# Kernel tuning notes

Measured on AMD Instinct MI355X. Metric: run time of the kernel, lower is better.

## Reference

```python
import jax, jax.numpy as jnp
import numpy as np

NUM_HEADS = 16
MAX_BATCH = 4
MAX_SEQ = 2048


def setup_inputs() -> dict:
    key = jax.random.key(0)
    ks = jax.random.split(key, 9)
    B, S, H = 4, 2048, 2048
    scale = 0.02
    hidden_state = jax.random.normal(ks[0], (B, S, H), dtype=jnp.float32)
    # causal mask (masked_fill where mask == 0), broadcastable over batch/heads
    mask = jnp.tril(jnp.ones((S, S), dtype=jnp.int32))[None, None]  # [1,1,S,S]
    Wq = jax.random.normal(ks[1], (H, H), dtype=jnp.float32) * scale
    Wk = jax.random.normal(ks[2], (H, H), dtype=jnp.float32) * scale
    Wv = jax.random.normal(ks[3], (H, H), dtype=jnp.float32) * scale
    Wo = jax.random.normal(ks[4], (H, H), dtype=jnp.float32) * scale
    bq = jax.random.normal(ks[5], (H,), dtype=jnp.float32) * scale
    bk = jax.random.normal(ks[6], (H,), dtype=jnp.float32) * scale
    bv = jax.random.normal(ks[7], (H,), dtype=jnp.float32) * scale
    bo = jax.random.normal(ks[8], (H,), dtype=jnp.float32) * scale
    return {"hidden_state": hidden_state, "mask": mask,
            "Wq": Wq, "bq": bq, "Wk": Wk, "bk": bk,
            "Wv": Wv, "bv": bv, "Wo": Wo, "bo": bo,
            "start_pos": 0}


def reference(hidden_state, mask, Wq, bq, Wk, bk, Wv, bv, Wo, bo, start_pos):
    B, S, H = hidden_state.shape
    nh = NUM_HEADS
    hd = H // nh
    # qkv projections (nn.Linear: x @ W.T + b)
    q = (hidden_state @ Wq.T + bq).reshape(B, S, nh, hd)
    k = (hidden_state @ Wk.T + bk).reshape(B, S, nh, hd)
    v = (hidden_state @ Wv.T + bv).reshape(B, S, nh, hd)
    # KV-cache append (zeros-initialized buffer, write [start_pos:start_pos+S])
    cache_k = jnp.zeros((MAX_BATCH, MAX_SEQ, nh, hd), dtype=q.dtype)
    cache_v = jnp.zeros((MAX_BATCH, MAX_SEQ, nh, hd), dtype=q.dtype)
    cache_k = jax.lax.dynamic_update_slice(cache_k, k, (0, start_pos, 0, 0))
    cache_v = jax.lax.dynamic_update_slice(cache_v, v, (0, start_pos, 0, 0))
    total = start_pos + S
    key = cache_k[:B, :total]   # [B, total, nh, hd]
    value = cache_v[:B, :total]
    # scores: [B, nh, S, total]
    scores = jnp.einsum('bqhd,bkhd->bhqk', q, key) / jnp.sqrt(jnp.float32(hd))
    scores = jnp.where(mask == 0, -jnp.inf, scores)
    probs = jax.nn.softmax(scores, axis=-1)
    out = jnp.einsum('bhqk,bkhd->bqhd', probs, value).reshape(B, S, H)
    return out @ Wo.T + bo
```

## Files before the change

kernel.cpp:

```cpp
#include <hip/hip_runtime.h>
#include <hip/hip_bf16.h>
#include <stdint.h>

#define S_LEN 2048
#define HDIM  2048
#define NH    16
#define HD    128
#define BATCH 4

typedef __attribute__((ext_vector_type(8))) short bf16x8;
typedef __attribute__((ext_vector_type(4))) float f32x4;
typedef __attribute__((ext_vector_type(4))) float float4v;
typedef __attribute__((ext_vector_type(4))) unsigned short u16x4;

__device__ __forceinline__ void gload_lds16(const void* g, void* l) {
  __builtin_amdgcn_global_load_lds(
      (const __attribute__((address_space(1))) unsigned int*)g,
      (__attribute__((address_space(3))) unsigned int*)l,
      16, 0, 0);
}

__device__ __forceinline__ unsigned short f2bf(float x) {
  __hip_bfloat16 b = __float2bfloat16(x);
  return *reinterpret_cast<unsigned short*>(&b);
}

#define SL2E 0.1275174465f

__global__ __launch_bounds__(256) void cvt5_kernel(
    const float* __restrict__ x,
    const float* __restrict__ w0, const float* __restrict__ w1,
    const float* __restrict__ w2, const float* __restrict__ w3,
    unsigned short* __restrict__ ox,
    unsigned short* __restrict__ o0, unsigned short* __restrict__ o1,
    unsigned short* __restrict__ o2, unsigned short* __restrict__ o3,
    int n4x, int n4w) {
  const int y = blockIdx.y;
  const float* in = (y == 0) ? x : (y == 1) ? w0 : (y == 2) ? w1 : (y == 3) ? w2 : w3;
  unsigned short* out = (y == 0) ? ox : (y == 1) ? o0 : (y == 2) ? o1 : (y == 3) ? o2 : o3;
  const int n4 = (y == 0) ? n4x : n4w;
  int stride = gridDim.x * blockDim.x;
  for (int i = blockIdx.x * blockDim.x + threadIdx.x; i < n4; i += stride) {
    float4v v = *(const float4v*)(in + (size_t)i * 4);
    u16x4 o;
    o.x = f2bf(v.x); o.y = f2bf(v.y); o.z = f2bf(v.z); o.w = f2bf(v.w);
    *(u16x4*)(out + (size_t)i * 4) = o;
  }
}


#define G8_VMW(N) asm volatile("s_waitcnt vmcnt(" #N ")" ::: "memory")
#define G8_BAR1() do { __builtin_amdgcn_sched_barrier(0); __builtin_amdgcn_s_barrier(); \
  asm volatile("s_waitcnt lgkmcnt(0)" ::: "memory"); __builtin_amdgcn_sched_barrier(0); } while (0)
#define G8_BAR2() do { __builtin_amdgcn_sched_barrier(0); __builtin_amdgcn_s_barrier(); \
  __builtin_amdgcn_sched_barrier(0); } while (0)

#define G8_STAGE(ISB, BUF, HALF, KT) do {                                          \
  int kt_ = (KT); if (kt_ > nkt1) kt_ = nkt1;                                      \
  const char* gs_ = ((ISB) ? Bg : Ag) +                                            \
      (size_t)(((ISB) ? bn : bm) * 256 + (HALF) * 128 + w * 16) * (size_t)K2 +     \
      (size_t)kt_ * 128;                                                           \
  char* ld_ = lds + (BUF) * 65536 + (ISB) * 32768 + ((HALF) * 128 + w * 16) * 128; \
  gload_lds16(gs_ + sLn, ld_);                                                     \
  gload_lds16(gs_ + 8 * (size_t)K2 + sLn, ld_ + 1024);                             \
} while (0)

#define G8_RDA(BUF, MI0) do {                                                      \
  _Pragma("unroll") for (int mi = 0; mi < 4; ++mi)                                 \
  _Pragma("unroll") for (int kk = 0; kk < 2; ++kk)                                 \
    a[mi][kk] = *(const bf16x8*)(lds + (BUF) * 65536 +                             \
        (wm + ((MI0) + mi) * 16 + ln) * 128 + ((((kk << 2) + g) ^ ln7) << 4));     \
} while (0)

#define G8_RDB(BUF, NI0, BREG) do {                                                \
  _Pragma("unroll") for (int ni = 0; ni < 2; ++ni)                                 \
  _Pragma("unroll") for (int kk = 0; kk < 2; ++kk)                                 \
    BREG[ni][kk] = *(const bf16x8*)(lds + (BUF) * 65536 + 32768 +                  \
        (wn + ((NI0) + ni) * 16 + ln) * 128 + ((((kk << 2) + g) ^ ln7) << 4));     \
} while (0)

#define G8_MFMA(M0, N0, BREG) do {                                                 \
  __builtin_amdgcn_s_setprio(1);                                                   \
  _Pragma("unroll") for (int mi = 0; mi < 4; ++mi)                                 \
  _Pragma("unroll") for (int ni = 0; ni < 2; ++ni)                                 \
  _Pragma("unroll") for (int kk = 0; kk < 2; ++kk)                                 \
    acc[(M0) + mi][(N0) + ni] = __builtin_amdgcn_mfma_f32_16x16x32_bf16(           \
        a[mi][kk], BREG[ni][kk], acc[(M0) + mi][(N0) + ni], 0, 0, 0);              \
  __builtin_amdgcn_s_setprio(0);                                                   \
} while (0)

#define G8_MAIN_LOOP() do {                                                        \
  G8_STAGE(0, 0, 0, 0); G8_STAGE(0, 0, 1, 0);                                      \
  G8_STAGE(1, 0, 0, 0); G8_STAGE(1, 0, 1, 0);                                      \
  G8_STAGE(1, 1, 0, 1); G8_STAGE(1, 1, 1, 1);                                      \
  G8_VMW(4);                                                                       \
  G8_BAR2();                                                                       \
  for (int i = 0; i < niter; ++i) {                                                \
    const int v = 2 * i + 1, u2 = 2 * i + 2, v2 = 2 * i + 3;                       \
    bf16x8 a[4][2], b0[2][2], b1[2][2];                                            \
    G8_RDA(0, 0); G8_RDB(0, 0, b0);                                                \
    G8_STAGE(0, 1, 0, v);                                                          \
    G8_BAR1(); G8_MFMA(0, 0, b0); G8_BAR2();                                       \
    G8_RDB(0, 2, b1);                                                              \
    G8_STAGE(0, 1, 1, v);                                                          \
    G8_BAR1(); G8_MFMA(0, 2, b1); G8_BAR2();                                       \
    G8_RDA(0, 4);                                                                  \
    G8_STAGE(1, 0, 0, u2);                                                         \
    G8_BAR1(); G8_MFMA(4, 0, b0); G8_BAR2();                                       \
    G8_STAGE(1, 0, 1, u2);                                                         \
    G8_VMW(4);                                                                     \
    G8_BAR1(); G8_MFMA(4, 2, b1); G8_BAR2();                                       \
    G8_RDA(1, 0); G8_RDB(1, 0, b0);                                                \
    G8_STAGE(0, 0, 0, u2);                                                         \
    G8_BAR1(); G8_MFMA(0, 0, b0); G8_BAR2();                                       \
    G8_RDB(1, 2, b1);                                                              \
    G8_STAGE(0, 0, 1, u2);                                                         \
    G8_BAR1(); G8_MFMA(0, 2, b1); G8_BAR2();                                       \
    G8_RDA(1, 4);                                                                  \
    G8_STAGE(1, 1, 0, v2);                                                         \
    G8_BAR1(); G8_MFMA(4, 0, b0); G8_BAR2();                                       \
    G8_STAGE(1, 1, 1, v2);                                                         \
    G8_VMW(4);                                                                     \
    G8_BAR1(); G8_MFMA(4, 2, b1); G8_BAR2();                                       \
  }                                                                                \
  G8_VMW(0);                                                                       \
} while (0)

__global__ __launch_bounds__(512, 2) void gemm8_qkv(
    const __hip_bfloat16* __restrict__ A,
    const __hip_bfloat16* __restrict__ Bq, const __hip_bfloat16* __restrict__ Bk,
    const __hip_bfloat16* __restrict__ Bv,
    const float* __restrict__ biasq, const float* __restrict__ biask,
    const float* __restrict__ biasv,
    __hip_bfloat16* __restrict__ Cq, __hip_bfloat16* __restrict__ Ck,
    __hip_bfloat16* __restrict__ Cv,
    int M, int N, int K) {
  __shared__ char lds[131072];
  const int tid = threadIdx.x;
  const int w = tid >> 6;
  const int lane = tid & 63;
  const int g = lane >> 4;
  const int ln = lane & 15;
  const int ln7 = lane & 7;
  const int K2 = K * 2;
  const int nkt = K >> 6;
  const int nkt1 = nkt - 1;
  const int niter = nkt >> 1;

  const int proj = blockIdx.x >> 8;
  const int bid  = blockIdx.x & 255;
  const int NBN = N >> 8;
  const int cpx = ((M >> 8) * NBN) >> 3;
  const int wg = (bid & 7) * cpx + (bid >> 3);
  const int bm = wg / NBN, bn = wg % NBN;

  const int wm = (w >> 2) * 128;
  const int wn = (w & 3) * 64;

  const char* Ag = (const char*)A;
  const char* Bg = (proj == 0) ? (const char*)Bq : (proj == 1) ? (const char*)Bk
                                                               : (const char*)Bv;
  const float* bias = (proj == 0) ? biasq : (proj == 1) ? biask : biasv;
  const float scale = (proj == 0) ? SL2E : 1.0f;
  const size_t sLn = (size_t)(lane >> 3) * (size_t)K2 +
                     (size_t)(((lane & 7) ^ (lane >> 3)) << 4);

  f32x4 acc[8][4];
#pragma unroll
  for (int mi = 0; mi < 8; ++mi)
#pragma unroll
    for (int ni = 0; ni < 4; ++ni) acc[mi][ni] = (f32x4){0.f, 0.f, 0.f, 0.f};

  G8_MAIN_LOOP();

#pragma unroll
  for (int ni = 0; ni < 4; ++ni) {
    const int col = bn * 256 + wn + ni * 16 + ln;
    const float bv = bias[col];
#pragma unroll
    for (int mi = 0; mi < 8; ++mi) {
      const int row0 = bm * 256 + wm + mi * 16 + g * 4;
      if (proj == 2) {
        const int h = col >> 7, d = col & 127;
        const size_t base = ((size_t)((row0 >> 11) * NH + h) * HD + d) * S_LEN +
                            (row0 & (S_LEN - 1));
        u16x4 pk;
#pragma unroll
        for (int r = 0; r < 4; ++r) pk[r] = f2bf(acc[mi][ni][r] + bv);
        *(u16x4*)((unsigned short*)Cv + base) = pk;
      } else {
        __hip_bfloat16* C = (proj == 0) ? Cq : Ck;
#pragma unroll
        for (int r = 0; r < 4; ++r)
          C[(size_t)(row0 + r) * N + col] = __float2bfloat16((acc[mi][ni][r] + bv) * scale);
      }
    }
  }
}

template<int OUTMODE>
__global__ __launch_bounds__(512, 2) void gemm8(
    const __hip_bfloat16* __restrict__ A, const __hip_bfloat16* __restrict__ B,
    const float* __restrict__ bias, void* __restrict__ C,
    int M, int N, int K, float scale) {
  __shared__ char lds[131072];
  const int tid = threadIdx.x;
  const int w = tid >> 6;
  const int lane = tid & 63;
  const int g = lane >> 4;
  const int ln = lane & 15;
  const int ln7 = lane & 7;
  const int K2 = K * 2;
  const int nkt = K >> 6;
  const int nkt1 = nkt - 1;
  const int niter = nkt >> 1;

  const int NBN = N >> 8;
  const int nwg = (M >> 8) * NBN;
  const int cpx = nwg >> 3;
  const int bid = blockIdx.x;
  const int wg = (bid & 7) * cpx + (bid >> 3);
  const int bm = wg / NBN, bn = wg % NBN;

  const int wm = (w >> 2) * 128;
  const int wn = (w & 3) * 64;

  const char* Ag = (const char*)A;
  const char* Bg = (const char*)B;
  const size_t sLn = (size_t)(lane >> 3) * (size_t)K2 +
                     (size_t)(((lane & 7) ^ (lane >> 3)) << 4);

  f32x4 acc[8][4];
#pragma unroll
  for (int mi = 0; mi < 8; ++mi)
#pragma unroll
    for (int ni = 0; ni < 4; ++ni) acc[mi][ni] = (f32x4){0.f, 0.f, 0.f, 0.f};

  G8_MAIN_LOOP();

#pragma unroll
  for (int ni = 0; ni < 4; ++ni) {
    const int col = bn * 256 + wn + ni * 16 + ln;
    const float bv = bias[col];
#pragma unroll
    for (int mi = 0; mi < 8; ++mi) {
      const int row0 = bm * 256 + wm + mi * 16 + g * 4;
#pragma unroll
      for (int r = 0; r < 4; ++r) {
        float val = (acc[mi][ni][r] + bv) * scale;
        if (OUTMODE == 1)
          ((float*)C)[(size_t)(row0 + r) * N + col] = val;
        else
          ((__hip_bfloat16*)C)[(size_t)(row0 + r) * N + col] = __float2bfloat16(val);
      }
    }
  }
}

#define DEFER_THR 8.0f

__global__ __launch_bounds__(256, 2) void attn_kernel(
    const __hip_bfloat16* __restrict__ Q, const __hip_bfloat16* __restrict__ Kg,
    const __hip_bfloat16* __restrict__ Vt, __hip_bfloat16* __restrict__ O) {
  __shared__ char lds[49152];
  const int tid = threadIdx.x;
  const int w = tid >> 6;
  const int lane = tid & 63;
  const int g = lane >> 4;
  const int ln = lane & 15;
  const int bh = blockIdx.x;
  const int pairid = blockIdx.y;
  const int b = bh >> 4, h = bh & 15;

  const char* Qb = (const char*)Q + ((size_t)b * S_LEN * HDIM + h * HD) * 2;
  const char* Kb = (const char*)Kg + ((size_t)b * S_LEN * HDIM + h * HD) * 2;
  const char* Vb = (const char*)Vt + ((size_t)bh * HD * S_LEN) * 2;
  char* ldsK = lds;
  char* ldsV = lds + 16384;
  char* pw   = lds + 32768 + w * 4096;

  const int kr = lane >> 4;
  const int kc = lane & 15;
  const int vr = lane >> 3;
  const int vc = lane & 7;

  auto stage = [&](int kv0) {
#pragma unroll
    for (int i = 0; i < 4; i++) {
      int r = w * 16 + i * 4 + kr;
      gload_lds16(Kb + (size_t)(kv0 + r) * (HDIM * 2) + ((kc ^ (r & 7)) << 4),
                  ldsK + (w * 16 + i * 4) * 256);
    }
#pragma unroll
    for (int i = 0; i < 4; i++) {
      int r = w * 32 + i * 8 + vr;
      gload_lds16(Vb + (size_t)r * (S_LEN * 2) + (size_t)kv0 * 2 + ((vc ^ vr) << 4),
                  ldsV + (w * 32 + i * 8) * 128);
    }
  };

  for (int pass = 0; pass < 2; pass++) {
    const int qt = pass == 0 ? (15 - pairid) : pairid;
    const int q0 = qt * 128 + w * 32;

    const int nt = 2 * qt + 2;
    __syncthreads();
    stage(0);

    bf16x8 qf[2][4];
#pragma unroll
    for (int qs = 0; qs < 2; qs++)
#pragma unroll
      for (int dc = 0; dc < 4; dc++)
        qf[qs][dc] = *(const bf16x8*)(Qb + (size_t)(q0 + qs * 16 + ln) * HDIM * 2 +
                                      (dc * 32 + g * 8) * 2);

    f32x4 o[2][8];
#pragma unroll
    for (int qs = 0; qs < 2; qs++)
#pragma unroll
      for (int ds = 0; ds < 8; ds++) o[qs][ds] = (f32x4){0.f, 0.f, 0.f, 0.f};
    float mrun[2][4], lrun[2][4];
#pragma unroll
    for (int qs = 0; qs < 2; qs++)
#pragma unroll
      for (int r = 0; r < 4; r++) { mrun[qs][r] = -__builtin_inff(); lrun[qs][r] = 0.f; }

    __syncthreads();

    for (int t = 0; t < nt; t++) {
      const int kv0 = t * 64;

      if (kv0 <= q0 + 31) {
        f32x4 sa[2][4];
#pragma unroll
        for (int qs = 0; qs < 2; qs++)
#pragma unroll
          for (int ks = 0; ks < 4; ks++) sa[qs][ks] = (f32x4){0.f, 0.f, 0.f, 0.f};
#pragma unroll
        for (int dc = 0; dc < 4; dc++) {
          bf16x8 kf[4];
#pragma unroll
          for (int ks = 0; ks < 4; ks++)
            kf[ks] = *(const bf16x8*)(ldsK + (ks * 16 + ln) * 256 +
                                      (((dc * 4 + g) ^ (ln & 7)) << 4));
          __builtin_amdgcn_s_setprio(1);
#pragma unroll
          for (int qs = 0; qs < 2; qs++)
#pragma unroll
            for (int ks = 0; ks < 4; ks++)
              sa[qs][ks] = __builtin_amdgcn_mfma_f32_16x16x32_bf16(qf[qs][dc], kf[ks], sa[qs][ks], 0, 0, 0);
          __builtin_amdgcn_s_setprio(0);
        }
        const bool needmask = (kv0 + 63) > q0;
        if (needmask) {
#pragma unroll
          for (int qs = 0; qs < 2; qs++)
#pragma unroll
            for (int ks = 0; ks < 4; ks++)
#pragma unroll
              for (int r = 0; r < 4; r++)
                if ((kv0 + ks * 16 + ln) > (q0 + qs * 16 + g * 4 + r))
                  sa[qs][ks][r] = -__builtin_inff();
        }
        float pmax[2][4];
#pragma unroll
        for (int qs = 0; qs < 2; qs++)
#pragma unroll
          for (int r = 0; r < 4; r++) {
            float mx = fmaxf(fmaxf(sa[qs][0][r], sa[qs][1][r]), fmaxf(sa[qs][2][r], sa[qs][3][r]));
            mx = fmaxf(mx, __shfl_xor(mx, 1));
            mx = fmaxf(mx, __shfl_xor(mx, 2));
            mx = fmaxf(mx, __shfl_xor(mx, 4));
            mx = fmaxf(mx, __shfl_xor(mx, 8));
            pmax[qs][r] = mx;
          }
        float dmin = 1e30f;
#pragma unroll
        for (int qs = 0; qs < 2; qs++)
#pragma unroll
          for (int r = 0; r < 4; r++)
            dmin = fminf(dmin, mrun[qs][r] + DEFER_THR - pmax[qs][r]);
        if (!__all(dmin >= 0.0f)) {
          float alpha[2][4];
#pragma unroll
          for (int qs = 0; qs < 2; qs++)
#pragma unroll
            for (int r = 0; r < 4; r++) {
              float mn = fmaxf(mrun[qs][r], pmax[qs][r]);
              alpha[qs][r] = exp2f(mrun[qs][r] - mn);
              mrun[qs][r] = mn;
              lrun[qs][r] *= alpha[qs][r];
            }
#pragma unroll
          for (int qs = 0; qs < 2; qs++)
#pragma unroll
            for (int ds = 0; ds < 8; ds++)
#pragma unroll
              for (int r = 0; r < 4; r++) o[qs][ds][r] *= alpha[qs][r];
        }
        float rsum[2][4];
#pragma unroll
        for (int qs = 0; qs < 2; qs++)
#pragma unroll
          for (int r = 0; r < 4; r++) rsum[qs][r] = 0.f;
#pragma unroll
        for (int qs = 0; qs < 2; qs++)
#pragma unroll
          for (int ks = 0; ks < 4; ks++)
#pragma unroll
            for (int r = 0; r < 4; r++) {
              float p = exp2f(sa[qs][ks][r] - mrun[qs][r]);
              sa[qs][ks][r] = p;
              rsum[qs][r] += p;
            }
#pragma unroll
        for (int qs = 0; qs < 2; qs++)
#pragma unroll
          for (int r = 0; r < 4; r++) {
            float rs = rsum[qs][r];
            rs += __shfl_xor(rs, 1);
            rs += __shfl_xor(rs, 2);
            rs += __shfl_xor(rs, 4);
            rs += __shfl_xor(rs, 8);
            lrun[qs][r] += rs;
          }
#pragma unroll
        for (int qs = 0; qs < 2; qs++)
#pragma unroll
          for (int ks = 0; ks < 4; ks++)
#pragma unroll
            for (int r = 0; r < 4; r++) {
              int row = qs * 16 + g * 4 + r;
              int key = ks * 16 + ln;
              *(__hip_bfloat16*)(pw + row * 128 + (((key >> 3) ^ (row & 7)) << 4) + (key & 7) * 2) =
                  __float2bfloat16(sa[qs][ks][r]);
            }
#pragma unroll
        for (int kk = 0; kk < 2; kk++) {
          bf16x8 pa[2];
#pragma unroll
          for (int qs = 0; qs < 2; qs++) {
            int row = qs * 16 + ln;
            pa[qs] = *(const bf16x8*)(pw + row * 128 + (((kk * 4 + g) ^ (row & 7)) << 4));
          }
          __builtin_amdgcn_s_setprio(1);
#pragma unroll
          for (int ds = 0; ds < 8; ds++) {
            bf16x8 vf = *(const bf16x8*)(ldsV + (ds * 16 + ln) * 128 +
                                         (((kk * 4 + g) ^ (ln & 7)) << 4));
#pragma unroll
            for (int qs = 0; qs < 2; qs++)
              o[qs][ds] = __builtin_amdgcn_mfma_f32_16x16x32_bf16(pa[qs], vf, o[qs][ds], 0, 0, 0);
          }
          __builtin_amdgcn_s_setprio(0);
        }
      }

      if (t + 1 < nt) {
        __syncthreads();
        stage(kv0 + 64);
        __syncthreads();
      }
    }
    float inv[2][4];
#pragma unroll
    for (int qs = 0; qs < 2; qs++)
#pragma unroll
      for (int r = 0; r < 4; r++) inv[qs][r] = 1.0f / lrun[qs][r];
    __hip_bfloat16* Ob = O + (size_t)b * S_LEN * HDIM + h * HD;
#pragma unroll
    for (int qs = 0; qs < 2; qs++)
#pragma unroll
      for (int ds = 0; ds < 8; ds++)
#pragma unroll
        for (int r = 0; r < 4; r++)
          Ob[(size_t)(q0 + qs * 16 + g * 4 + r) * HDIM + ds * 16 + ln] =
              __float2bfloat16(o[qs][ds][r] * inv[qs][r]);
  }
}

extern "C" void kernel_launch(void* const* d_in, const int* in_sizes, int n_in,
                              void* d_out, int out_size, void* d_ws, size_t ws_size,
                              hipStream_t stream) {
  const float* X  = (const float*)d_in[0];
  const float* Wq = (const float*)d_in[2];
  const float* bq = (const float*)d_in[3];
  const float* Wk = (const float*)d_in[4];
  const float* bk = (const float*)d_in[5];
  const float* Wv = (const float*)d_in[6];
  const float* bv = (const float*)d_in[7];
  const float* Wo = (const float*)d_in[8];
  const float* bo = (const float*)d_in[9];

  char* ws = (char*)d_ws;
  __hip_bfloat16* Xb   = (__hip_bfloat16*)(ws);
  __hip_bfloat16* Wqb  = (__hip_bfloat16*)(ws + 33554432);
  __hip_bfloat16* Wkb  = (__hip_bfloat16*)(ws + 41943040);
  __hip_bfloat16* Wvb  = (__hip_bfloat16*)(ws + 50331648);
  __hip_bfloat16* Wob  = (__hip_bfloat16*)(ws + 58720256);
  __hip_bfloat16* Qb   = (__hip_bfloat16*)(ws + 67108864);
  __hip_bfloat16* Kb   = (__hip_bfloat16*)(ws + 100663296);
  __hip_bfloat16* Ob   = (__hip_bfloat16*)(ws + 134217728);
  __hip_bfloat16* Vtb  = (__hip_bfloat16*)(ws + 167772160);

  cvt5_kernel<<<dim3(512, 5), 256, 0, stream>>>(
      X, Wq, Wk, Wv, Wo,
      (unsigned short*)Xb,
      (unsigned short*)Wqb, (unsigned short*)Wkb,
      (unsigned short*)Wvb, (unsigned short*)Wob,
      16777216 / 4, 4194304 / 4);

  gemm8_qkv<<<768, 512, 0, stream>>>(Xb, Wqb, Wkb, Wvb, bq, bk, bv,
                                     Qb, Kb, Vtb, 8192, 2048, 2048);

  attn_kernel<<<dim3(64, 8), 256, 0, stream>>>(Qb, Kb, Vtb, Ob);

  gemm8<1><<<256, 512, 0, stream>>>(Ob, Wob, bo, (float*)d_out, 8192, 2048, 2048, 1.0f);
}
```

Before: 433.4 us.

## Double-buffer K/V tiles in LDS and prefetch the next tile during compute

Splits the K and V LDS regions into two buffers and issues the async global-to-LDS loads for tile t+1 at the start of iteration t. Compute then reads the current buffer, so the two barriers around each staging step become one barrier per iteration. The per-wave P scratch is shrunk to a 32-key slice, written and read once per kk half with a new swizzle, which frees LDS for the second buffer. Total LDS per block grows to 72 KB, which still fits two blocks per CU but leaves less slack. Correctness depends on the end-of-iteration barrier waiting for the outstanding LDS-DMA loads.

Result: no change. 438.5 us (+1.2%).

```diff
diff --git a/kernel.cpp b/kernel.cpp
--- a/kernel.cpp
+++ b/kernel.cpp
@@ -258,11 +258,12 @@
 }
 
 #define DEFER_THR 8.0f
+#define PSWZ(row) ((((row) & 3) ^ (((row) >> 2) & 3)))
 
 __global__ __launch_bounds__(256, 2) void attn_kernel(
     const __hip_bfloat16* __restrict__ Q, const __hip_bfloat16* __restrict__ Kg,
     const __hip_bfloat16* __restrict__ Vt, __hip_bfloat16* __restrict__ O) {
-  __shared__ char lds[49152];
+  __shared__ char lds[73728];
   const int tid = threadIdx.x;
   const int w = tid >> 6;
   const int lane = tid & 63;
@@ -276,26 +277,26 @@
   const char* Kb = (const char*)Kg + ((size_t)b * S_LEN * HDIM + h * HD) * 2;
   const char* Vb = (const char*)Vt + ((size_t)bh * HD * S_LEN) * 2;
   char* ldsK = lds;
-  char* ldsV = lds + 16384;
-  char* pw   = lds + 32768 + w * 4096;
+  char* ldsV = lds + 32768;
+  char* pw   = lds + 65536 + w * 2048;
 
   const int kr = lane >> 4;
   const int kc = lane & 15;
   const int vr = lane >> 3;
   const int vc = lane & 7;
 
-  auto stage = [&](int kv0) {
+  auto stage = [&](int buf, int kv0) {
 #pragma unroll
     for (int i = 0; i < 4; i++) {
       int r = w * 16 + i * 4 + kr;
       gload_lds16(Kb + (size_t)(kv0 + r) * (HDIM * 2) + ((kc ^ (r & 7)) << 4),
-                  ldsK + (w * 16 + i * 4) * 256);
+                  ldsK + buf * 16384 + (w * 16 + i * 4) * 256);
     }
 #pragma unroll
     for (int i = 0; i < 4; i++) {
       int r = w * 32 + i * 8 + vr;
       gload_lds16(Vb + (size_t)r * (S_LEN * 2) + (size_t)kv0 * 2 + ((vc ^ vr) << 4),
-                  ldsV + (w * 32 + i * 8) * 128);
+                  ldsV + buf * 16384 + (w * 32 + i * 8) * 128);
     }
   };
 
@@ -304,8 +305,7 @@
     const int q0 = qt * 128 + w * 32;
 
     const int nt = 2 * qt + 2;
-    __syncthreads();
-    stage(0);
+    stage(0, 0);
 
     bf16x8 qf[2][4];
 #pragma unroll
@@ -330,6 +330,8 @@
 
     for (int t = 0; t < nt; t++) {
       const int kv0 = t * 64;
+      const int buf = t & 1;
+      if (t + 1 < nt) stage((t + 1) & 1, kv0 + 64);
 
       if (kv0 <= q0 + 31) {
         f32x4 sa[2][4];
@@ -342,7 +344,7 @@
           bf16x8 kf[4];
 #pragma unroll
           for (int ks = 0; ks < 4; ks++)
-            kf[ks] = *(const bf16x8*)(ldsK + (ks * 16 + ln) * 256 +
+            kf[ks] = *(const bf16x8*)(ldsK + buf * 16384 + (ks * 16 + ln) * 256 +
                                       (((dc * 4 + g) ^ (ln & 7)) << 4));
           __builtin_amdgcn_s_setprio(1);
 #pragma unroll
@@ -426,28 +428,29 @@
             lrun[qs][r] += rs;
           }
 #pragma unroll
-        for (int qs = 0; qs < 2; qs++)
-#pragma unroll
-          for (int ks = 0; ks < 4; ks++)
-#pragma unroll
-            for (int r = 0; r < 4; r++) {
-              int row = qs * 16 + g * 4 + r;
-              int key = ks * 16 + ln;
-              *(__hip_bfloat16*)(pw + row * 128 + (((key >> 3) ^ (row & 7)) << 4) + (key & 7) * 2) =
-                  __float2bfloat16(sa[qs][ks][r]);
-            }
-#pragma unroll
         for (int kk = 0; kk < 2; kk++) {
+#pragma unroll
+          for (int qs = 0; qs < 2; qs++)
+#pragma unroll
+            for (int ki = 0; ki < 2; ki++)
+#pragma unroll
+              for (int r = 0; r < 4; r++) {
+                int row = qs * 16 + g * 4 + r;
+                int lk  = ki * 16 + ln;
+                *(__hip_bfloat16*)(pw + row * 64 +
+                    ((((lk >> 3) & 3) ^ PSWZ(row)) << 4) + (lk & 7) * 2) =
+                    __float2bfloat16(sa[qs][2 * kk + ki][r]);
+              }
           bf16x8 pa[2];
 #pragma unroll
           for (int qs = 0; qs < 2; qs++) {
             int row = qs * 16 + ln;
-            pa[qs] = *(const bf16x8*)(pw + row * 128 + (((kk * 4 + g) ^ (row & 7)) << 4));
+            pa[qs] = *(const bf16x8*)(pw + row * 64 + ((g ^ PSWZ(row)) << 4));
           }
           __builtin_amdgcn_s_setprio(1);
 #pragma unroll
           for (int ds = 0; ds < 8; ds++) {
-            bf16x8 vf = *(const bf16x8*)(ldsV + (ds * 16 + ln) * 128 +
+            bf16x8 vf = *(const bf16x8*)(ldsV + buf * 16384 + (ds * 16 + ln) * 128 +
                                          (((kk * 4 + g) ^ (ln & 7)) << 4));
 #pragma unroll
             for (int qs = 0; qs < 2; qs++)
@@ -457,11 +460,7 @@
         }
       }
 
-      if (t + 1 < nt) {
-        __syncthreads();
-        stage(kv0 + 64);
-        __syncthreads();
-      }
+      __syncthreads();
     }
     float inv[2][4];
 #pragma unroll
```
